# Kernel tuning notes

Hardware: AMD Instinct MI355X
Metric: run time of the kernel (lower is better)

The kernel has to match this reference:

```python
import jax, jax.numpy as jnp
import numpy as np

B, S, M, D = 16, 64, 2048, 256
TOPK = 8  # min(8, memory_size)


def setup_inputs() -> dict:
    key = jax.random.key(0)
    ks = jax.random.split(key, 8)
    s = 0.02
    return {
        "x": jax.random.normal(ks[0], (B, S, D), dtype=jnp.float32),
        "memory": jax.random.normal(ks[1], (M, D), dtype=jnp.float32),
        "Wq": jax.random.normal(ks[2], (D, D), dtype=jnp.float32) * s,
        "bq": jnp.zeros((D,), jnp.float32),
        "Wk": jax.random.normal(ks[3], (D, D), dtype=jnp.float32) * s,
        "bk": jnp.zeros((D,), jnp.float32),
        "Wv": jax.random.normal(ks[4], (D, D), dtype=jnp.float32) * s,
        "bv": jnp.zeros((D,), jnp.float32),
        "Wu": jax.random.normal(ks[5], (D, 2 * D), dtype=jnp.float32) * s,
        "bu": jnp.zeros((D,), jnp.float32),
    }


def reference(x, memory, Wq, bq, Wk, bk, Wv, bv, Wu, bu):
    Bsz, S_, D_ = x.shape
    scale = 1.0 / jnp.sqrt(jnp.asarray(D_, x.dtype))
    # per-batch copy of the memory bank, mutated across timesteps
    mem0 = jnp.broadcast_to(memory, (Bsz,) + memory.shape).astype(x.dtype)

    def step(mem, xt):
        # mem: [B, M, D], xt: [B, D]
        q = xt @ Wq.T + bq                                    # [B, D]
        k = mem @ Wk.T + bk                                   # [B, M, D]
        v = mem @ Wv.T + bv                                   # [B, M, D]
        attn = jax.nn.softmax(jnp.einsum('bd,bmd->bm', q, k) * scale, axis=-1)
        mem_out = jnp.einsum('bm,bmd->bd', attn, v)           # [B, D]
        gate = jax.nn.sigmoid(jnp.concatenate([xt, mem_out], axis=-1) @ Wu.T + bu)  # [B, D]
        _, idx = jax.lax.top_k(attn, TOPK)                    # [B, TOPK] int32, distinct
        gathered = jnp.take_along_axis(mem, idx[:, :, None], axis=1)  # [B, TOPK, D]
        updated = (1.0 - gate)[:, None, :] * gathered + gate[:, None, :] * xt[:, None, :]
        mem = jax.vmap(lambda m, i, u: m.at[i].set(u))(mem, idx, updated)
        return mem, mem_out

    _, outs = jax.lax.scan(step, mem0, jnp.swapaxes(x, 0, 1))  # outs: [S, B, D]
    return jnp.swapaxes(outs, 0, 1)                            # [B, S, D]
```

## Files before the change

### kernel.cpp

```cpp
#include <hip/hip_runtime.h>
#include <math.h>

#define BB 16
#define SS 64
#define MM 2048
#define DD 256
#define TOPK 8
#define NCH 16
#define CHR 128
#define SCALE 0.0625f

__device__ __forceinline__ float wave_sum(float p) {
    for (int o = 32; o; o >>= 1) p += __shfl_xor(p, o);
    return p;
}

__device__ __forceinline__ void wave_argmax(float& v, int& i) {
    for (int o = 32; o; o >>= 1) {
        float ov = __shfl_xor(v, o);
        int oi = __shfl_xor(i, o);
        if (ov > v || (ov == v && oi < i)) { v = ov; i = oi; }
    }
}

__device__ __forceinline__ void astf(float* p, float v) {
    __hip_atomic_store(p, v, __ATOMIC_RELAXED, __HIP_MEMORY_SCOPE_AGENT);
}
__device__ __forceinline__ float aldf(const float* p) {
    return __hip_atomic_load(p, __ATOMIC_RELAXED, __HIP_MEMORY_SCOPE_AGENT);
}
__device__ __forceinline__ void asti(int* p, int v) {
    __hip_atomic_store(p, v, __ATOMIC_RELAXED, __HIP_MEMORY_SCOPE_AGENT);
}
__device__ __forceinline__ int aldi(const int* p) {
    return __hip_atomic_load(p, __ATOMIC_RELAXED, __HIP_MEMORY_SCOPE_AGENT);
}

__global__ __launch_bounds__(256) void k_tr(const float* __restrict__ src, float* __restrict__ dst,
                                            int sld, int dld) {
    __shared__ float ts[32][33];
    int c0 = blockIdx.x * 32, r0 = blockIdx.y * 32;
    int xx = threadIdx.x & 31, yy = threadIdx.x >> 5;
    for (int i = 0; i < 4; ++i)
        ts[yy + 8 * i][xx] = src[(size_t)(r0 + yy + 8 * i) * sld + c0 + xx];
    __syncthreads();
    for (int i = 0; i < 4; ++i)
        dst[(size_t)(c0 + yy + 8 * i) * dld + r0 + xx] = ts[xx][yy + 8 * i];
}

__global__ __launch_bounds__(256) void k_gemv(const float* __restrict__ A, const float* __restrict__ B,
                                              const float* __restrict__ bias, float* __restrict__ C,
                                              const float* __restrict__ bkv, float* __restrict__ c0o) {
    const int i = blockIdx.x, tid = threadIdx.x;
    __shared__ float as[DD];
    as[tid] = A[(size_t)i * DD + tid];
    __syncthreads();
    float a0 = bias ? bias[tid] : 0.f, a1 = 0.f;
#pragma unroll 4
    for (int d = 0; d < DD; d += 2) {
        a0 = fmaf(as[d],     B[(size_t)d * DD + tid],       a0);
        a1 = fmaf(as[d + 1], B[(size_t)(d + 1) * DD + tid], a1);
    }
    C[(size_t)i * DD + tid] = a0 + a1;
    if (c0o && tid < 64) {
        float4 a4 = ((const float4*)as)[tid];
        float4 b4 = ((const float4*)bkv)[tid];
        float p = wave_sum(a4.x * b4.x + a4.y * b4.y + a4.z * b4.z + a4.w * b4.w);
        if (tid == 0) c0o[i] = p;
    }
}

__global__ __launch_bounds__(256) void k_fuse(const float* __restrict__ Wu, const float* __restrict__ Wv,
                                              const float* __restrict__ bv, float* __restrict__ F,
                                              float* __restrict__ cb) {
    const int j = blockIdx.x, tid = threadIdx.x;
    const float* wuh = Wu + (size_t)j * (2 * DD) + DD;
    float a0 = 0.f, a1 = 0.f;
#pragma unroll 4
    for (int k = 0; k < DD; k += 2) {
        a0 = fmaf(wuh[k],     Wv[(size_t)k * DD + tid],       a0);
        a1 = fmaf(wuh[k + 1], Wv[(size_t)(k + 1) * DD + tid], a1);
    }
    F[(size_t)j * DD + tid] = a0 + a1;
    if (tid < 64) {
        float4 b4 = ((const float4*)bv)[tid];
        float4 w4 = ((const float4*)wuh)[tid];
        float p = wave_sum(b4.x * w4.x + b4.y * w4.y + b4.z * w4.z + b4.w * w4.w);
        if (tid == 0) cb[j] = p;
    }
}

__global__ __launch_bounds__(256) void k_zero(int* __restrict__ p, int n) {
    int i = blockIdx.x * 256 + threadIdx.x;
    if (i < n) p[i] = 0;
}

__device__ __forceinline__ void batch_barrier(unsigned* c, unsigned target) {
    __syncthreads();
    if (threadIdx.x == 0) {
        asm volatile("s_waitcnt vmcnt(0)" ::: "memory");
        __hip_atomic_fetch_add(c, 1u, __ATOMIC_RELAXED, __HIP_MEMORY_SCOPE_AGENT);
        while (__hip_atomic_load(c, __ATOMIC_RELAXED, __HIP_MEMORY_SCOPE_AGENT) < target)
            __builtin_amdgcn_s_sleep(1);
        asm volatile("" ::: "memory");
    }
    __syncthreads();
}

__global__ __launch_bounds__(1024) void k_persist(
    const float* __restrict__ x, const float* __restrict__ memory0,
    const float* __restrict__ memT, const float* __restrict__ QK,
    const float* __restrict__ c0All, const float* __restrict__ GXU,
    const float* __restrict__ F, const float* __restrict__ cb,
    const float* __restrict__ Wv, const float* __restrict__ bv,
    float* __restrict__ dval, float* __restrict__ pe2, float* __restrict__ pam2,
    float* __restrict__ candV2, int* __restrict__ candI2, float* __restrict__ gGlob,
    int* __restrict__ flagslot, int* __restrict__ listChunk,
    int* __restrict__ chunkCnt, int* __restrict__ slotCnt,
    unsigned* __restrict__ ctr, float* __restrict__ out) {
    const int c = blockIdx.x >> 4, b = blockIdx.x & 15;
    const int tid = threadIdx.x, w = tid >> 6, lane = tid & 63;
    const int col = tid & 255, q = tid >> 8;
    __shared__ float qks[DD], xs[DD], amS[DD], gs[DD];
    __shared__ float es[CHR];
    __shared__ float pPart[8][CHR];
    __shared__ float cPart[4][DD];
    __shared__ float peS[16];
    __shared__ int topI[TOPK];
    __shared__ int slotArr[TOPK], wasArr[TOPK];
    unsigned* myctr = ctr + b * 16;
    unsigned barTarget = 0;

    for (int t = 0; t < SS; ++t) {
        const int bt = (b << 6) + t;
        const int par = t & 1;
        float* peP    = pe2   + (size_t)par * BB * 16;
        float* pamP   = pam2  + (size_t)par * BB * 16 * DD;
        float* candVP = candV2 + (size_t)par * BB * 128;
        int*   candIP = candI2 + (size_t)par * BB * 128;

        if (tid < DD) {
            qks[tid] = QK[(size_t)bt * DD + tid];
            xs[tid]  = x[(size_t)bt * DD + tid];
        }
        const float c0v = c0All[bt];
        const int nd = aldi(&chunkCnt[b * 16 + c]);
        __syncthreads();

        {
            const int r = ((w & 1) << 6) + lane, ds = w >> 1;
            const float* mptr = memT + (size_t)(ds * 32) * MM + c * CHR + r;
            const float* qp = qks + ds * 32;
            float a0 = 0.f, a1 = 0.f, a2 = 0.f, a3 = 0.f;
#pragma unroll
            for (int d = 0; d < 32; d += 4) {
                a0 = fmaf(qp[d],     mptr[(size_t)d * MM],       a0);
                a1 = fmaf(qp[d + 1], mptr[(size_t)(d + 1) * MM], a1);
                a2 = fmaf(qp[d + 2], mptr[(size_t)(d + 2) * MM], a2);
                a3 = fmaf(qp[d + 3], mptr[(size_t)(d + 3) * MM], a3);
            }
            pPart[ds][r] = (a0 + a1) + (a2 + a3);
        }
        __syncthreads();
        if (tid < CHR) {
            float s = 0.f;
#pragma unroll
            for (int ds = 0; ds < 8; ++ds) s += pPart[ds][tid];
            es[tid] = expf((s + c0v) * SCALE);
        }
        __syncthreads();
        for (int i = w; i < nd; i += 16) {
            int packed = listChunk[(b * 16 + c) * CHR + i];
            int rl = packed & 127, slot = packed >> 7;
            float4 dv = ((const float4*)(dval + ((size_t)b * 512 + slot) * DD))[lane];
            float4 q4 = ((const float4*)qks)[lane];
            float p = wave_sum(dv.x * q4.x + dv.y * q4.y + dv.z * q4.z + dv.w * q4.w);
            if (lane == 0) es[rl] = expf((p + c0v) * SCALE);
        }
        __syncthreads();

        {
            const float* m0 = memory0 + ((size_t)c * CHR + q * 32) * DD + col;
            const float* eq = es + q * 32;
            float p = 0.f;
#pragma unroll 8
            for (int r = 0; r < 32; ++r) p = fmaf(eq[r], m0[(size_t)r * DD], p);
            for (int i = q; i < nd; i += 4) {
                int packed = listChunk[(b * 16 + c) * CHR + i];
                int rl = packed & 127, slot = packed >> 7;
                float e = es[rl];
                p += e * (dval[((size_t)b * 512 + slot) * DD + col]
                          - memory0[((size_t)c * CHR + rl) * DD + col]);
            }
            cPart[q][col] = p;
        }
        __syncthreads();
        if (tid < DD)
            astf(&pamP[(size_t)(b * 16 + c) * DD + tid],
                 cPart[0][tid] + cPart[1][tid] + cPart[2][tid] + cPart[3][tid]);
        if (w == 12) {
            float p = wave_sum(es[lane] + es[lane + 64]);
            if (lane == 0) astf(&peP[b * 16 + c], p);
        } else if (w == 13) {
            float v0 = es[lane], v1 = es[lane + 64];
            int i0 = lane, i1 = lane + 64;
            for (int k = 0; k < TOPK; ++k) {
                float bb = v0; int bi = i0;
                if (v1 > v0 || (v1 == v0 && i1 < i0)) { bb = v1; bi = i1; }
                wave_argmax(bb, bi);
                if (lane == 0) {
                    astf(&candVP[b * 128 + c * TOPK + k], bb);
                    asti(&candIP[b * 128 + c * TOPK + k], c * CHR + bi);
                }
                if (i0 == bi) v0 = -1e30f;
                if (i1 == bi) v1 = -1e30f;
            }
        }

        barTarget += 16;
        batch_barrier(myctr, barTarget);

        if (tid < 16) peS[tid] = aldf(&peP[b * 16 + tid]);
        {
            float a = 0.f;
#pragma unroll
            for (int p2 = q * 4; p2 < q * 4 + 4; ++p2)
                a += aldf(&pamP[(size_t)(b * 16 + p2) * DD + col]);
            cPart[q][col] = a;
        }
        __syncthreads();
        if (tid < DD) {
            float tot = 0.f;
#pragma unroll
            for (int i2 = 0; i2 < 16; ++i2) tot += peS[i2];
            amS[tid] = (cPart[0][tid] + cPart[1][tid] + cPart[2][tid] + cPart[3][tid]) / tot;
        }
        __syncthreads();
        {
            const int j = c * 16 + w;
            float4 a4 = ((const float4*)amS)[lane];
            float4 f4 = ((const float4*)(F + (size_t)j * DD))[lane];
            float pg = wave_sum(f4.x * a4.x + f4.y * a4.y + f4.z * a4.z + f4.w * a4.w);
            float4 w4 = ((const float4*)(Wv + (size_t)j * DD))[lane];
            float pv = wave_sum(w4.x * a4.x + w4.y * a4.y + w4.z * a4.z + w4.w * a4.w);
            if (lane == 0) {
                astf(&gGlob[b * DD + j],
                     1.f / (1.f + expf(-(pg + GXU[(size_t)bt * DD + j] + cb[j]))));
                out[(size_t)bt * DD + j] = pv + bv[j];
            }
        }
        if (w == 0) {
            float v0 = aldf(&candVP[b * 128 + lane]), v1 = aldf(&candVP[b * 128 + 64 + lane]);
            int i0 = aldi(&candIP[b * 128 + lane]), i1 = aldi(&candIP[b * 128 + 64 + lane]);
            for (int k = 0; k < TOPK; ++k) {
                float bb = v0; int bi = i0;
                if (v1 > v0 || (v1 == v0 && i1 < i0)) { bb = v1; bi = i1; }
                wave_argmax(bb, bi);
                if (lane == 0) topI[k] = bi;
                if (i0 == bi) v0 = -1e30f;
                if (i1 == bi) v1 = -1e30f;
            }
        }

        barTarget += 16;
        batch_barrier(myctr, barTarget);

        if (tid < DD) gs[tid] = aldf(&gGlob[b * DD + tid]);
        if (w == 0 && lane < TOPK) {
            int row = topI[lane];
            if ((row >> 7) == c) {
                int fs = flagslot[b * MM + row];
                int slot, wd = (fs != 0);
                if (!wd) {
                    slot = atomicAdd(&slotCnt[b], 1);
                    flagslot[b * MM + row] = slot + 1;
                    int cc = atomicAdd(&chunkCnt[b * 16 + c], 1);
                    listChunk[(b * 16 + c) * CHR + cc] = (slot << 7) | (row & 127);
                } else slot = fs - 1;
                slotArr[lane] = slot; wasArr[lane] = wd;
            }
        }
        __syncthreads();
        {
            float xv = xs[col], gv = gs[col];
#pragma unroll
            for (int kk = q; kk < TOPK; kk += 4) {
                int row = topI[kk];
                if ((row >> 7) == c) {
                    size_t doff = ((size_t)b * 512 + slotArr[kk]) * DD + col;
                    float gathered = wasArr[kk] ? dval[doff]
                                               : memory0[(size_t)row * DD + col];
                    dval[doff] = (1.f - gv) * gathered + gv * xv;
                }
            }
        }
        __syncthreads();
    }
}

extern "C" void kernel_launch(void* const* d_in, const int* in_sizes, int n_in,
                              void* d_out, int out_size, void* d_ws, size_t ws_size,
                              hipStream_t stream) {
    const float* x      = (const float*)d_in[0];
    const float* memory = (const float*)d_in[1];
    const float* Wq     = (const float*)d_in[2];
    const float* bq     = (const float*)d_in[3];
    const float* Wk     = (const float*)d_in[4];
    const float* bk     = (const float*)d_in[5];
    const float* Wv     = (const float*)d_in[6];
    const float* bv     = (const float*)d_in[7];
    const float* Wu     = (const float*)d_in[8];
    const float* bu     = (const float*)d_in[9];
    float* out = (float*)d_out;

    float* ws = (float*)d_ws;
    size_t o = 0;
    float* memT  = ws + o; o += (size_t)DD * MM;
    float* WqT   = ws + o; o += DD * DD;
    float* WulT  = ws + o; o += DD * DD;
    float* F     = ws + o; o += DD * DD;
    float* cbv   = ws + o; o += DD;
    float* Q     = ws + o; o += (size_t)BB * SS * DD;
    float* QK    = ws + o; o += (size_t)BB * SS * DD;
    float* GXU   = ws + o; o += (size_t)BB * SS * DD;
    float* c0All = ws + o; o += BB * SS;
    float* dval  = ws + o; o += (size_t)BB * 512 * DD;
    float* pe2   = ws + o; o += 2 * BB * 16;
    float* pam2  = ws + o; o += (size_t)2 * BB * 16 * DD;
    float* candV2 = ws + o; o += 2 * BB * 128;
    float* gGlob  = ws + o; o += BB * DD;
    int* candI2    = (int*)(ws + o); o += 2 * BB * 128;
    int* zbase     = (int*)(ws + o);
    int* flagslot  = (int*)(ws + o); o += BB * MM;
    int* listChunk = (int*)(ws + o); o += BB * 16 * CHR;
    int* chunkCnt  = (int*)(ws + o); o += BB * 16;
    int* slotCnt   = (int*)(ws + o); o += BB;
    unsigned* ctr  = (unsigned*)(ws + o); o += BB * 16;
    const int nzero = BB * MM + BB * 16 * CHR + BB * 16 + BB + BB * 16;

    k_tr<<<dim3(DD / 32, MM / 32), 256, 0, stream>>>(memory, memT, DD, MM);
    k_tr<<<dim3(DD / 32, DD / 32), 256, 0, stream>>>(Wq, WqT, DD, DD);
    k_tr<<<dim3(DD / 32, DD / 32), 256, 0, stream>>>(Wu, WulT, 2 * DD, DD);
    k_gemv<<<BB * SS, 256, 0, stream>>>(x, WqT, bq, Q, nullptr, nullptr);
    k_gemv<<<BB * SS, 256, 0, stream>>>(Q, Wk, nullptr, QK, bk, c0All);
    k_gemv<<<BB * SS, 256, 0, stream>>>(x, WulT, bu, GXU, nullptr, nullptr);
    k_fuse<<<DD, 256, 0, stream>>>(Wu, Wv, bv, F, cbv);
    k_zero<<<(nzero + 255) / 256, 256, 0, stream>>>(zbase, nzero);
    k_persist<<<BB * NCH, 1024, 0, stream>>>(x, memory, memT, QK, c0All, GXU, F, cbv,
                                             Wv, bv, dval, pe2, pam2, candV2, candI2, gGlob,
                                             flagslot, listChunk, chunkCnt, slotCnt, ctr, out);
}
```

Before: 1.296 ms.

## Precompute base attention scores and drop second per-step batch barrier

Adds a batched kernel that computes the dot products of every query-key with the original memory bank for all timesteps ahead of time, so the persistent kernel only reads and exponentiates a precomputed score instead of recomputing a 256-long dot product per row per step. The gate and output projections are restructured so that only chunk blocks owning a top-k row compute the gate locally (redundantly), and only chunk 0 writes the output. This removes the gGlob exchange and the second cross-block barrier per timestep. The cost is a large extra scratch buffer and redundant gate computation in owner blocks.

```diff
diff --git a/kernel.cpp b/kernel.cpp
--- a/kernel.cpp
+++ b/kernel.cpp
@@ -90,6 +90,32 @@
     }
 }
 
+__global__ __launch_bounds__(1024) void k_sbase(const float* __restrict__ QK,
+                                                const float* __restrict__ memT,
+                                                float* __restrict__ Sbase) {
+    const int tid = threadIdx.x;
+    const int mloc = tid & 255, bs = tid >> 8;
+    const int m0 = blockIdx.x * 256, bt0 = blockIdx.y * 16;
+    __shared__ float qkS[16][DD];
+    for (int i = tid; i < 16 * DD; i += 1024)
+        ((float*)qkS)[i] = QK[(size_t)bt0 * DD + i];
+    __syncthreads();
+    float acc0 = 0.f, acc1 = 0.f, acc2 = 0.f, acc3 = 0.f;
+    const float* mp = memT + m0 + mloc;
+    const int r0 = bs * 4;
+#pragma unroll 4
+    for (int d = 0; d < DD; ++d) {
+        float v = mp[(size_t)d * MM];
+        acc0 = fmaf(qkS[r0][d],     v, acc0);
+        acc1 = fmaf(qkS[r0 + 1][d], v, acc1);
+        acc2 = fmaf(qkS[r0 + 2][d], v, acc2);
+        acc3 = fmaf(qkS[r0 + 3][d], v, acc3);
+    }
+    size_t ob = (size_t)(bt0 + r0) * MM + m0 + mloc;
+    Sbase[ob] = acc0; Sbase[ob + MM] = acc1;
+    Sbase[ob + 2 * MM] = acc2; Sbase[ob + 3 * MM] = acc3;
+}
+
 __global__ __launch_bounds__(256) void k_zero(int* __restrict__ p, int n) {
     int i = blockIdx.x * 256 + threadIdx.x;
     if (i < n) p[i] = 0;
@@ -109,12 +135,12 @@
 
 __global__ __launch_bounds__(1024) void k_persist(
     const float* __restrict__ x, const float* __restrict__ memory0,
-    const float* __restrict__ memT, const float* __restrict__ QK,
+    const float* __restrict__ Sbase, const float* __restrict__ QK,
     const float* __restrict__ c0All, const float* __restrict__ GXU,
     const float* __restrict__ F, const float* __restrict__ cb,
     const float* __restrict__ Wv, const float* __restrict__ bv,
     float* __restrict__ dval, float* __restrict__ pe2, float* __restrict__ pam2,
-    float* __restrict__ candV2, int* __restrict__ candI2, float* __restrict__ gGlob,
+    float* __restrict__ candV2, int* __restrict__ candI2,
     int* __restrict__ flagslot, int* __restrict__ listChunk,
     int* __restrict__ chunkCnt, int* __restrict__ slotCnt,
     unsigned* __restrict__ ctr, float* __restrict__ out) {
@@ -123,7 +149,6 @@
     const int col = tid & 255, q = tid >> 8;
     __shared__ float qks[DD], xs[DD], amS[DD], gs[DD];
     __shared__ float es[CHR];
-    __shared__ float pPart[8][CHR];
     __shared__ float cPart[4][DD];
     __shared__ float peS[16];
     __shared__ int topI[TOPK];
@@ -134,8 +159,8 @@
     for (int t = 0; t < SS; ++t) {
         const int bt = (b << 6) + t;
         const int par = t & 1;
-        float* peP    = pe2   + (size_t)par * BB * 16;
-        float* pamP   = pam2  + (size_t)par * BB * 16 * DD;
+        float* peP    = pe2    + (size_t)par * BB * 16;
+        float* pamP   = pam2   + (size_t)par * BB * 16 * DD;
         float* candVP = candV2 + (size_t)par * BB * 128;
         int*   candIP = candI2 + (size_t)par * BB * 128;
 
@@ -145,30 +170,10 @@
         }
         const float c0v = c0All[bt];
         const int nd = aldi(&chunkCnt[b * 16 + c]);
-        __syncthreads();
-
-        {
-            const int r = ((w & 1) << 6) + lane, ds = w >> 1;
-            const float* mptr = memT + (size_t)(ds * 32) * MM + c * CHR + r;
-            const float* qp = qks + ds * 32;
-            float a0 = 0.f, a1 = 0.f, a2 = 0.f, a3 = 0.f;
-#pragma unroll
-            for (int d = 0; d < 32; d += 4) {
-                a0 = fmaf(qp[d],     mptr[(size_t)d * MM],       a0);
-                a1 = fmaf(qp[d + 1], mptr[(size_t)(d + 1) * MM], a1);
-                a2 = fmaf(qp[d + 2], mptr[(size_t)(d + 2) * MM], a2);
-                a3 = fmaf(qp[d + 3], mptr[(size_t)(d + 3) * MM], a3);
-            }
-            pPart[ds][r] = (a0 + a1) + (a2 + a3);
-        }
-        __syncthreads();
-        if (tid < CHR) {
-            float s = 0.f;
-#pragma unroll
-            for (int ds = 0; ds < 8; ++ds) s += pPart[ds][tid];
-            es[tid] = expf((s + c0v) * SCALE);
-        }
-        __syncthreads();
+        if (tid < CHR)
+            es[tid] = expf((Sbase[(size_t)bt * MM + c * CHR + tid] + c0v) * SCALE);
+        __syncthreads();
+
         for (int i = w; i < nd; i += 16) {
             int packed = listChunk[(b * 16 + c) * CHR + i];
             int rl = packed & 127, slot = packed >> 7;
@@ -220,7 +225,6 @@
         barTarget += 16;
         batch_barrier(myctr, barTarget);
 
-        if (tid < 16) peS[tid] = aldf(&peP[b * 16 + tid]);
         {
             float a = 0.f;
 #pragma unroll
@@ -228,26 +232,14 @@
                 a += aldf(&pamP[(size_t)(b * 16 + p2) * DD + col]);
             cPart[q][col] = a;
         }
-        __syncthreads();
-        if (tid < DD) {
+        if (tid < 16) peS[tid] = aldf(&peP[b * 16 + tid]);
+        __syncthreads();
+        if (w >= 4 && w < 8) {
+            int d = tid - 256;
             float tot = 0.f;
 #pragma unroll
             for (int i2 = 0; i2 < 16; ++i2) tot += peS[i2];
-            amS[tid] = (cPart[0][tid] + cPart[1][tid] + cPart[2][tid] + cPart[3][tid]) / tot;
-        }
-        __syncthreads();
-        {
-            const int j = c * 16 + w;
-            float4 a4 = ((const float4*)amS)[lane];
-            float4 f4 = ((const float4*)(F + (size_t)j * DD))[lane];
-            float pg = wave_sum(f4.x * a4.x + f4.y * a4.y + f4.z * a4.z + f4.w * a4.w);
-            float4 w4 = ((const float4*)(Wv + (size_t)j * DD))[lane];
-            float pv = wave_sum(w4.x * a4.x + w4.y * a4.y + w4.z * a4.z + w4.w * a4.w);
-            if (lane == 0) {
-                astf(&gGlob[b * DD + j],
-                     1.f / (1.f + expf(-(pg + GXU[(size_t)bt * DD + j] + cb[j]))));
-                out[(size_t)bt * DD + j] = pv + bv[j];
-            }
+            amS[d] = (cPart[0][d] + cPart[1][d] + cPart[2][d] + cPart[3][d]) / tot;
         }
         if (w == 0) {
             float v0 = aldf(&candVP[b * 128 + lane]), v1 = aldf(&candVP[b * 128 + 64 + lane]);
@@ -261,36 +253,57 @@
                 if (i1 == bi) v1 = -1e30f;
             }
         }
-
-        barTarget += 16;
-        batch_barrier(myctr, barTarget);
-
-        if (tid < DD) gs[tid] = aldf(&gGlob[b * DD + tid]);
-        if (w == 0 && lane < TOPK) {
-            int row = topI[lane];
-            if ((row >> 7) == c) {
-                int fs = flagslot[b * MM + row];
-                int slot, wd = (fs != 0);
-                if (!wd) {
-                    slot = atomicAdd(&slotCnt[b], 1);
-                    flagslot[b * MM + row] = slot + 1;
-                    int cc = atomicAdd(&chunkCnt[b * 16 + c], 1);
-                    listChunk[(b * 16 + c) * CHR + cc] = (slot << 7) | (row & 127);
-                } else slot = fs - 1;
-                slotArr[lane] = slot; wasArr[lane] = wd;
-            }
-        }
-        __syncthreads();
-        {
-            float xv = xs[col], gv = gs[col];
+        __syncthreads();
+
+        bool owner = false;
 #pragma unroll
-            for (int kk = q; kk < TOPK; kk += 4) {
-                int row = topI[kk];
+        for (int k = 0; k < TOPK; ++k) owner |= ((topI[k] >> 7) == c);
+
+        if (c == 0) {
+            float4 a4 = ((const float4*)amS)[lane];
+            for (int i = 0; i < 16; ++i) {
+                int j = w * 16 + i;
+                float4 w4 = ((const float4*)(Wv + (size_t)j * DD))[lane];
+                float pv = wave_sum(w4.x * a4.x + w4.y * a4.y + w4.z * a4.z + w4.w * a4.w);
+                if (lane == 0) out[(size_t)bt * DD + j] = pv + bv[j];
+            }
+        }
+        if (owner) {
+            float4 a4 = ((const float4*)amS)[lane];
+            for (int i = 0; i < 16; ++i) {
+                int j = w * 16 + i;
+                float4 f4 = ((const float4*)(F + (size_t)j * DD))[lane];
+                float pg = wave_sum(f4.x * a4.x + f4.y * a4.y + f4.z * a4.z + f4.w * a4.w);
+                if (lane == 0)
+                    gs[j] = 1.f / (1.f + expf(-(pg + GXU[(size_t)bt * DD + j] + cb[j])));
+            }
+            __syncthreads();
+            if (w == 0 && lane < TOPK) {
+                int row = topI[lane];
                 if ((row >> 7) == c) {
-                    size_t doff = ((size_t)b * 512 + slotArr[kk]) * DD + col;
-                    float gathered = wasArr[kk] ? dval[doff]
-                                               : memory0[(size_t)row * DD + col];
-                    dval[doff] = (1.f - gv) * gathered + gv * xv;
+                    int fs = flagslot[b * MM + row];
+                    int slot, wd = (fs != 0);
+                    if (!wd) {
+                        slot = atomicAdd(&slotCnt[b], 1);
+                        flagslot[b * MM + row] = slot + 1;
+                        int cc = atomicAdd(&chunkCnt[b * 16 + c], 1);
+                        listChunk[(b * 16 + c) * CHR + cc] = (slot << 7) | (row & 127);
+                    } else slot = fs - 1;
+                    slotArr[lane] = slot; wasArr[lane] = wd;
+                }
+            }
+            __syncthreads();
+            {
+                float xv = xs[col], gv = gs[col];
+#pragma unroll
+                for (int kk = q; kk < TOPK; kk += 4) {
+                    int row = topI[kk];
+                    if ((row >> 7) == c) {
+                        size_t doff = ((size_t)b * 512 + slotArr[kk]) * DD + col;
+                        float gathered = wasArr[kk] ? dval[doff]
+                                                    : memory0[(size_t)row * DD + col];
+                        dval[doff] = (1.f - gv) * gathered + gv * xv;
+                    }
                 }
             }
         }
@@ -324,11 +337,11 @@
     float* QK    = ws + o; o += (size_t)BB * SS * DD;
     float* GXU   = ws + o; o += (size_t)BB * SS * DD;
     float* c0All = ws + o; o += BB * SS;
+    float* Sbase = ws + o; o += (size_t)BB * SS * MM;
     float* dval  = ws + o; o += (size_t)BB * 512 * DD;
     float* pe2   = ws + o; o += 2 * BB * 16;
     float* pam2  = ws + o; o += (size_t)2 * BB * 16 * DD;
     float* candV2 = ws + o; o += 2 * BB * 128;
-    float* gGlob  = ws + o; o += BB * DD;
     int* candI2    = (int*)(ws + o); o += 2 * BB * 128;
     int* zbase     = (int*)(ws + o);
     int* flagslot  = (int*)(ws + o); o += BB * MM;
@@ -345,8 +358,9 @@
     k_gemv<<<BB * SS, 256, 0, stream>>>(Q, Wk, nullptr, QK, bk, c0All);
     k_gemv<<<BB * SS, 256, 0, stream>>>(x, WulT, bu, GXU, nullptr, nullptr);
     k_fuse<<<DD, 256, 0, stream>>>(Wu, Wv, bv, F, cbv);
+    k_sbase<<<dim3(MM / 256, BB * SS / 16), 1024, 0, stream>>>(QK, memT, Sbase);
     k_zero<<<(nzero + 255) / 256, 256, 0, stream>>>(zbase, nzero);
-    k_persist<<<BB * NCH, 1024, 0, stream>>>(x, memory, memT, QK, c0All, GXU, F, cbv,
-                                             Wv, bv, dval, pe2, pam2, candV2, candI2, gGlob,
+    k_persist<<<BB * NCH, 1024, 0, stream>>>(x, memory, Sbase, QK, c0All, GXU, F, cbv,
+                                             Wv, bv, dval, pe2, pam2, candV2, candI2,
                                              flagslot, listChunk, chunkCnt, slotCnt, ctr, out);
 }
```

Result: slower. 1.877 ms (+44.9%).
